# Kernel optimization log

Measured on AMD Instinct MI355X. Metric: run time of the kernel, lower is better.

The kernel has to match this reference:

```python
import jax, jax.numpy as jnp
import numpy as np

N_NODES = 10000
N_EDGES = 160000
B = 128
HEADS = 4
DIMS = [36, 128, 256, 512]
NEG_SLOPE = 0.2  # PyG GATConv default


def setup_inputs() -> dict:
    key = jax.random.key(0)
    ks = jax.random.split(key, 32)
    inp = {}
    inp["x"] = jax.random.normal(ks[0], (N_NODES, DIMS[0]), jnp.float32)
    inp["edge_index"] = jax.random.randint(ks[1], (2, N_EDGES), 0, N_NODES)
    inp["batch"] = jnp.sort(jax.random.randint(ks[2], (N_NODES,), 0, B))
    ki = 3
    for i in range(3):
        din, dout = DIMS[i], DIMS[i + 1]
        C = dout // HEADS
        inp[f"gcn_w{i}"] = jax.random.normal(ks[ki], (din, dout), jnp.float32) * (din ** -0.5); ki += 1
        inp[f"gcn_b{i}"] = jnp.zeros((dout,), jnp.float32)
        inp[f"gat_w{i}"] = jax.random.normal(ks[ki], (dout, dout), jnp.float32) * (dout ** -0.5); ki += 1
        inp[f"gat_as{i}"] = jax.random.normal(ks[ki], (HEADS, C), jnp.float32) * 0.1; ki += 1
        inp[f"gat_ad{i}"] = jax.random.normal(ks[ki], (HEADS, C), jnp.float32) * 0.1; ki += 1
        inp[f"gat_b{i}"] = jnp.zeros((dout,), jnp.float32)
    D = DIMS[-1]
    inp["ap_w1"] = jax.random.normal(ks[ki], (D, D // 2), jnp.float32) * (D ** -0.5); ki += 1
    inp["ap_b1"] = jnp.zeros((D // 2,), jnp.float32)
    inp["ap_w2"] = jax.random.normal(ks[ki], (D // 2, 1), jnp.float32) * ((D // 2) ** -0.5); ki += 1
    inp["ap_b2"] = jnp.zeros((1,), jnp.float32)
    return inp


def _gcn(x, w, b, src, dst, n):
    # PyG GCNConv: add self-loops, symmetric deg^-1/2 normalization, bias after agg
    h = x @ w  # [N, dout]
    deg = jax.ops.segment_sum(jnp.ones_like(dst, dtype=h.dtype), dst, n) + 1.0  # incl. self-loop
    dinv = deg ** -0.5
    norm = dinv[src] * dinv[dst]  # [E]
    agg = jax.ops.segment_sum(h[src] * norm[:, None], dst, n)
    agg = agg + h * (dinv * dinv)[:, None]  # self-loop messages
    return agg + b


def _gat(x, w, a_s, a_d, b, src, dst, n):
    # PyG GATConv: self-loops, leaky-relu logits, segment softmax over dst, concat heads
    C = w.shape[1] // HEADS
    h = (x @ w).reshape(n, HEADS, C)
    alpha_src = (h * a_s).sum(-1)  # [N, H]
    alpha_dst = (h * a_d).sum(-1)  # [N, H]
    loop = jnp.arange(n)
    s = jnp.concatenate([src, loop])
    d = jnp.concatenate([dst, loop])
    e = jax.nn.leaky_relu(alpha_src[s] + alpha_dst[d], NEG_SLOPE)  # [E+N, H]
    m = jax.ops.segment_max(e, d, n)
    ex = jnp.exp(e - m[d])
    den = jax.ops.segment_sum(ex, d, n)
    alpha = ex / den[d]  # [E+N, H]
    out = jax.ops.segment_sum(h[s] * alpha[:, :, None], d, n)  # [N, H, C]
    return out.reshape(n, HEADS * C) + b


def _forward(x, edge_index, batch, params, ap_w1, ap_b1, ap_w2, ap_b2):
    src, dst = edge_index[0], edge_index[1]
    n = x.shape[0]
    x_in = x
    n_layers = len(params)
    for i, (gw, gb, aw, a_s, a_d, ab) in enumerate(params):
        h = jax.nn.relu(_gcn(x, gw, gb, src, dst, n))  # dropout is identity in eval
        x = h + _gat(h, aw, a_s, a_d, ab, src, dst, n)
        if i < n_layers - 1:
            if x.shape[-1] == x_in.shape[-1]:
                x = x + x_in
            x_in = x
    # attention pooling (global softmax then per-graph masked renorm)
    a = jnp.tanh(x @ ap_w1 + ap_b1) @ ap_w2 + ap_b2  # [N, 1]
    a = jax.nn.softmax(a, axis=0)
    mask = jax.nn.one_hot(batch, B, dtype=x.dtype)  # [N, B]
    aw_ = a * mask
    aw_ = aw_ / (aw_.sum(0, keepdims=True) + 1e-8)
    graph_emb = aw_.T @ x  # [B, D]
    cnt = jax.ops.segment_sum(jnp.ones((n,), x.dtype), batch, B)
    ssum = jax.ops.segment_sum(x, batch, B)
    mean = ssum / jnp.maximum(cnt, 1.0)[:, None]
    smax = jax.ops.segment_max(x, batch, B)
    return jnp.concatenate([graph_emb, mean, smax, ssum], axis=1)  # [B, 4*D]


def reference(x, edge_index, batch,
              gcn_w0, gcn_b0, gat_w0, gat_as0, gat_ad0, gat_b0,
              gcn_w1, gcn_b1, gat_w1, gat_as1, gat_ad1, gat_b1,
              gcn_w2, gcn_b2, gat_w2, gat_as2, gat_ad2, gat_b2,
              ap_w1, ap_b1, ap_w2, ap_b2):
    params = [
        (gcn_w0, gcn_b0, gat_w0, gat_as0, gat_ad0, gat_b0),
        (gcn_w1, gcn_b1, gat_w1, gat_as1, gat_ad1, gat_b1),
        (gcn_w2, gcn_b2, gat_w2, gat_as2, gat_ad2, gat_b2),
    ]
    return _forward(x, edge_index, batch, params, ap_w1, ap_b1, ap_w2, ap_b2)
```

## Files before the change

kernel.cpp:

```cpp
#include <hip/hip_runtime.h>
#include <math.h>

#define NN 10000
#define NE 160000
#define NB 128
#define NH 4
#define DOUT 512
#define NEG 0.2f
#define SCAN_BLKS ((NN + 255) / 256)

typedef __attribute__((ext_vector_type(8))) short short8;
typedef __attribute__((ext_vector_type(4))) float f32x4;
typedef __attribute__((ext_vector_type(4))) unsigned short us4;

__device__ __forceinline__ float leakyf(float v){ return v > 0.f ? v : NEG*v; }
__device__ __forceinline__ void fma4(float4& a, const float4 v, float w){
  a.x += v.x*w; a.y += v.y*w; a.z += v.z*w; a.w += v.w*w;
}
__device__ __forceinline__ void mul4(float4& a, float s){
  a.x *= s; a.y *= s; a.z *= s; a.w *= s;
}
__device__ __forceinline__ unsigned short f2bf(float f){
  unsigned int u = __float_as_uint(f);
  u += 0x7FFFu + ((u >> 16) & 1u);
  return (unsigned short)(u >> 16);
}
__device__ __forceinline__ float bf2f(unsigned short h){
  return __uint_as_float(((unsigned int)h) << 16);
}
__device__ __forceinline__ void split2(float v, unsigned short& h, unsigned short& l){
  h = f2bf(v);
  l = f2bf(v - bf2f(h));
}
__device__ __forceinline__ void store_hl(unsigned short* H, unsigned short* L,
                                         size_t base, float4 v){
  us4 h, l; unsigned short hh, ll;
  split2(v.x, hh, ll); h[0]=hh; l[0]=ll;
  split2(v.y, hh, ll); h[1]=hh; l[1]=ll;
  split2(v.z, hh, ll); h[2]=hh; l[2]=ll;
  split2(v.w, hh, ll); h[3]=hh; l[3]=ll;
  *(us4*)&H[base] = h;
  *(us4*)&L[base] = l;
}
__device__ __forceinline__ float4 load_hl(const unsigned short* __restrict__ H,
                                          const unsigned short* __restrict__ L, size_t base){
  us4 h = *(const us4*)&H[base];
  us4 l = *(const us4*)&L[base];
  return make_float4(bf2f(h[0])+bf2f(l[0]), bf2f(h[1])+bf2f(l[1]),
                     bf2f(h[2])+bf2f(l[2]), bf2f(h[3])+bf2f(l[3]));
}
__device__ __forceinline__ void gl_lds16(const unsigned short* g, unsigned short* l){
  __builtin_amdgcn_global_load_lds(
      (const __attribute__((address_space(1))) unsigned int*)g,
      (__attribute__((address_space(3))) unsigned int*)l, 16, 0, 0);
}

__global__ void k_count(const int* __restrict__ dst, int* __restrict__ cnt){
  int e = blockIdx.x*blockDim.x + threadIdx.x;
  if (e < NE) atomicAdd(&cnt[dst[e]], 1);
}
__global__ void k_scan1(const int* __restrict__ cnt, int* __restrict__ bsum,
                        const int* __restrict__ batch, int* __restrict__ starts){
  __shared__ int red[256];
  int blk = blockIdx.x, t = threadIdx.x;
  int idx = blk*256 + t;
  red[t] = (idx < NN) ? cnt[idx] : 0;
  __syncthreads();
  for (int o = 128; o > 0; o >>= 1){
    if (t < o) red[t] += red[t + o];
    __syncthreads();
  }
  if (t == 0) bsum[blk] = red[0];
  if (blk == 0 && t <= NB){
    int lo = 0, hi = NN;
    while (lo < hi){ int mid = (lo + hi) >> 1; if (batch[mid] < t) lo = mid + 1; else hi = mid; }
    starts[t] = lo;
  }
}
__global__ void k_scan2(int* __restrict__ bsum, int* __restrict__ rowptr){
  if (threadIdx.x == 0){
    int acc = 0;
    for (int i = 0; i < SCAN_BLKS; i++){
      int c = bsum[i]; bsum[i] = acc; acc += c;
    }
    rowptr[NN] = acc;
  }
}
__global__ void k_scan3(const int* __restrict__ cnt, const int* __restrict__ bsum,
                        int* __restrict__ rowptr, float* __restrict__ dinv,
                        int* __restrict__ cursor, float* __restrict__ apre){
  __shared__ int s[256];
  int blk = blockIdx.x, t = threadIdx.x;
  int idx = blk*256 + t;
  int c = (idx < NN) ? cnt[idx] : 0;
  s[t] = c; __syncthreads();
  for (int o = 1; o < 256; o <<= 1){
    int v = 0;
    if (t >= o) v = s[t - o];
    __syncthreads();
    if (t >= o) s[t] += v;
    __syncthreads();
  }
  if (idx < NN){
    rowptr[idx] = bsum[blk] + s[t] - c;
    dinv[idx] = rsqrtf((float)c + 1.f);
    cursor[idx] = 0;
    apre[idx] = 0.f;
  }
}
__global__ void k_fill(const int* __restrict__ src, const int* __restrict__ dst,
                       const int* __restrict__ rowptr, int* __restrict__ cursor,
                       int* __restrict__ colidx){
  int e = blockIdx.x*blockDim.x + threadIdx.x;
  if (e >= NE) return;
  int d = dst[e];
  int pos = atomicAdd(&cursor[d], 1);
  colidx[rowptr[d] + pos] = src[e];
}

struct AllConv {
  const float* src[8];
  unsigned short* dh[8];
  unsigned short* dl[8];
  int K[8], Mm[8], Kp[8], tot[8];
};
__global__ void k_convall(AllConv a){
  int j = blockIdx.y;
  int idx = blockIdx.x*blockDim.x + threadIdx.x;
  if (idx >= a.tot[j]) return;
  float v;
  if (j == 0){
    int n = idx >> 6, c = idx & 63;
    v = (c < 36) ? a.src[0][n*36 + c] : 0.f;
  } else {
    int Kp = a.Kp[j], K = a.K[j], M = a.Mm[j];
    int kk = idx % Kp, m = idx / Kp;
    v = (kk < K) ? a.src[j][(size_t)kk*M + m] : 0.f;
  }
  unsigned short h, l; split2(v, h, l);
  a.dh[j][idx] = h; a.dl[j][idx] = l;
}

#define GBM 64
#define GBN 128
#define GBK 32
__global__ __launch_bounds__(256) void k_gemm_bf3(
    const unsigned short* __restrict__ Ah, const unsigned short* __restrict__ Al,
    const unsigned short* __restrict__ Bh, const unsigned short* __restrict__ Bl,
    float* __restrict__ C, int N, int Kp, int M, int mode,
    const float* __restrict__ bias, unsigned short* __restrict__ outH,
    unsigned short* __restrict__ outL,
    const float* __restrict__ a_s, const float* __restrict__ a_d,
    float* __restrict__ as_o, float* __restrict__ ad_o, int Cdim){
  __shared__ unsigned short AsH[GBM*GBK], AsL[GBM*GBK];
  __shared__ unsigned short BsH[GBN*GBK], BsL[GBN*GBK];
  __shared__ float sred[2][GBM][4];
  int gx = M / GBN;
  int gy = (N + GBM - 1) / GBM;
  const int G = 8;
  int bid = blockIdx.x;
  int full = gy / G;
  int bid_full = full * G * gx;
  int by, bx;
  if (bid < bid_full){
    int g = bid / (G*gx); int rem = bid % (G*gx);
    by = g*G + rem % G; bx = rem / G;
  } else {
    int rem = bid - bid_full; int rows = gy - full*G;
    by = full*G + rem % rows; bx = rem / rows;
  }
  int row0 = by * GBM, col0 = bx * GBN;
  int t = threadIdx.x;
  int w = t >> 6, L = t & 63;
  int lm = L & 15, lq = L >> 4;
  int wc = w * 32;

  int sr = L >> 2, sc = L & 3;
  int art = w*16 + sr;
  int ga  = (sc - ((art >> 1) & 3)) & 3;
  int agrow = min(row0 + art, N-1);
  int brt0 = w*16 + sr;
  int brt1 = (w+4)*16 + sr;
  int gb0 = (sc - ((brt0 >> 1) & 3)) & 3;
  int gb1 = (sc - ((brt1 >> 1) & 3)) & 3;
  int bgrow0 = col0 + brt0, bgrow1 = col0 + brt1;

  int rc = (lq + (lm >> 1)) & 3;
  int aoff[4], boff[2];
#pragma unroll
  for (int mi = 0; mi < 4; mi++) aoff[mi] = (mi*16 + lm)*32 + rc*8;
#pragma unroll
  for (int ni = 0; ni < 2; ni++) boff[ni] = (wc + ni*16 + lm)*32 + rc*8;

  f32x4 acc[4][2];
#pragma unroll
  for (int i = 0; i < 4; i++)
#pragma unroll
    for (int j = 0; j < 2; j++) acc[i][j] = (f32x4){0.f,0.f,0.f,0.f};

  int nk = Kp / GBK;
  for (int kt = 0; kt < nk; kt++){
    int k0 = kt * GBK;
    if (kt) __syncthreads();
    gl_lds16(&Ah[(size_t)agrow*Kp + k0 + ga*8],  &AsH[w*512]);
    gl_lds16(&Al[(size_t)agrow*Kp + k0 + ga*8],  &AsL[w*512]);
    gl_lds16(&Bh[(size_t)bgrow0*Kp + k0 + gb0*8], &BsH[w*512]);
    gl_lds16(&Bh[(size_t)bgrow1*Kp + k0 + gb1*8], &BsH[(w+4)*512]);
    gl_lds16(&Bl[(size_t)bgrow0*Kp + k0 + gb0*8], &BsL[w*512]);
    gl_lds16(&Bl[(size_t)bgrow1*Kp + k0 + gb1*8], &BsL[(w+4)*512]);
    __syncthreads();

    short8 ah[4], al[4], bh[2], bl[2];
#pragma unroll
    for (int mi = 0; mi < 4; mi++){
      ah[mi] = *(const short8*)&AsH[aoff[mi]];
      al[mi] = *(const short8*)&AsL[aoff[mi]];
    }
#pragma unroll
    for (int ni = 0; ni < 2; ni++){
      bh[ni] = *(const short8*)&BsH[boff[ni]];
      bl[ni] = *(const short8*)&BsL[boff[ni]];
    }
#pragma unroll
    for (int mi = 0; mi < 4; mi++)
#pragma unroll
      for (int ni = 0; ni < 2; ni++){
        acc[mi][ni] = __builtin_amdgcn_mfma_f32_16x16x32_bf16(ah[mi], bh[ni], acc[mi][ni], 0, 0, 0);
        acc[mi][ni] = __builtin_amdgcn_mfma_f32_16x16x32_bf16(ah[mi], bl[ni], acc[mi][ni], 0, 0, 0);
        acc[mi][ni] = __builtin_amdgcn_mfma_f32_16x16x32_bf16(al[mi], bh[ni], acc[mi][ni], 0, 0, 0);
      }
  }
  if (mode == 1){
#pragma unroll
    for (int mi = 0; mi < 4; mi++)
#pragma unroll
      for (int ni = 0; ni < 2; ni++){
#pragma unroll
        for (int r = 0; r < 4; r++){
          int row = row0 + mi*16 + lq*4 + r;
          int col = col0 + wc + ni*16 + lm;
          if (row < N){
            float v = fmaxf(acc[mi][ni][r] + bias[col], 0.f);
            unsigned short hh, ll; split2(v, hh, ll);
            outH[(size_t)row*M + col] = hh;
            outL[(size_t)row*M + col] = ll;
          }
        }
      }
  } else if (mode != 3){
#pragma unroll
    for (int mi = 0; mi < 4; mi++)
#pragma unroll
      for (int ni = 0; ni < 2; ni++){
#pragma unroll
        for (int r = 0; r < 4; r++){
          int row = row0 + mi*16 + lq*4 + r;
          int col = col0 + wc + ni*16 + lm;
          if (row < N) C[(size_t)row*M + col] = acc[mi][ni][r];
        }
      }
  }
  if (mode == 2){
    float sA0 = a_s[col0 + wc + lm], sA1 = a_s[col0 + wc + 16 + lm];
    float dA0 = a_d[col0 + wc + lm], dA1 = a_d[col0 + wc + 16 + lm];
#pragma unroll
    for (int mi = 0; mi < 4; mi++)
#pragma unroll
      for (int r = 0; r < 4; r++){
        float vs = acc[mi][0][r]*sA0 + acc[mi][1][r]*sA1;
        float vd = acc[mi][0][r]*dA0 + acc[mi][1][r]*dA1;
#pragma unroll
        for (int o = 1; o <= 8; o <<= 1){
          vs += __shfl_xor(vs, o);
          vd += __shfl_xor(vd, o);
        }
        if (lm == 0){
          int row = mi*16 + lq*4 + r;
          sred[0][row][w] = vs;
          sred[1][row][w] = vd;
        }
      }
    __syncthreads();
    if (t < GBM){
      int n = row0 + t;
      if (n < N){
        int wph = Cdim >> 5;
        int nheads = 4 / wph;
        for (int g = 0; g < nheads; g++){
          float ss = 0.f, dd = 0.f;
          for (int q = 0; q < wph; q++){
            ss += sred[0][t][g*wph + q];
            dd += sred[1][t][g*wph + q];
          }
          int hd = (col0 + g*wph*32) / Cdim;
          as_o[n*NH + hd] = ss;
          ad_o[n*NH + hd] = dd;
        }
      }
    }
  } else if (mode == 3){
    float b0 = bias[col0 + wc + lm], b1v = bias[col0 + wc + 16 + lm];
    float w0v = a_s[col0 + wc + lm], w1v = a_s[col0 + wc + 16 + lm];
#pragma unroll
    for (int mi = 0; mi < 4; mi++)
#pragma unroll
      for (int r = 0; r < 4; r++){
        float v = tanhf(acc[mi][0][r] + b0)*w0v + tanhf(acc[mi][1][r] + b1v)*w1v;
#pragma unroll
        for (int o = 1; o <= 8; o <<= 1) v += __shfl_xor(v, o);
        if (lm == 0) sred[0][mi*16 + lq*4 + r][w] = v;
      }
    __syncthreads();
    if (t < GBM){
      int n = row0 + t;
      if (n < N){
        float s = sred[0][t][0] + sred[0][t][1] + sred[0][t][2] + sred[0][t][3];
        atomicAdd(&as_o[n], s);
      }
    }
  }
}

__global__ __launch_bounds__(256) void k_gcn_pre(
    const unsigned short* __restrict__ inH, const unsigned short* __restrict__ inL,
    const float* __restrict__ dinv,
    const int* __restrict__ rowptr, const int* __restrict__ colidx,
    unsigned short* __restrict__ outH, unsigned short* __restrict__ outL,
    int Kp, int nchunk){
  int bid = blockIdx.x;
  int chunk = bid % nchunk, grp = bid / nchunk;
  int t = threadIdx.x;
  int sub = t & 15;
  int n = grp*16 + (t >> 4);
  if (n >= NN) return;
  int f0 = chunk*64 + sub*4;
  int b = rowptr[n], e = rowptr[n+1];
  float dn = dinv[n];
  float4 a0 = make_float4(0,0,0,0), a1 = make_float4(0,0,0,0);
  float4 a2 = make_float4(0,0,0,0), a3 = make_float4(0,0,0,0);
  int j = b;
  for (; j + 3 < e; j += 4){
    int s0 = colidx[j], s1 = colidx[j+1], s2 = colidx[j+2], s3 = colidx[j+3];
    float w0 = dinv[s0], w1 = dinv[s1], w2 = dinv[s2], w3 = dinv[s3];
    float4 v0 = load_hl(inH, inL, (size_t)s0*Kp + f0);
    float4 v1 = load_hl(inH, inL, (size_t)s1*Kp + f0);
    float4 v2 = load_hl(inH, inL, (size_t)s2*Kp + f0);
    float4 v3 = load_hl(inH, inL, (size_t)s3*Kp + f0);
    fma4(a0, v0, w0*dn); fma4(a1, v1, w1*dn);
    fma4(a2, v2, w2*dn); fma4(a3, v3, w3*dn);
  }
  for (; j < e; j++){
    int s = colidx[j];
    float4 v = load_hl(inH, inL, (size_t)s*Kp + f0);
    fma4(a0, v, dinv[s]*dn);
  }
  float4 acc = make_float4(a0.x+a1.x+a2.x+a3.x, a0.y+a1.y+a2.y+a3.y,
                           a0.z+a1.z+a2.z+a3.z, a0.w+a1.w+a2.w+a3.w);
  float4 sv = load_hl(inH, inL, (size_t)n*Kp + f0);
  float dn2 = dn*dn;
  acc.x += sv.x*dn2; acc.y += sv.y*dn2; acc.z += sv.z*dn2; acc.w += sv.w*dn2;
  store_hl(outH, outL, (size_t)n*Kp + f0, acc);
}

__global__ __launch_bounds__(256) void k_gat_gather(
    const float* __restrict__ hg,
    const unsigned short* __restrict__ inH, const unsigned short* __restrict__ inL,
    const int* __restrict__ rowptr, const int* __restrict__ colidx,
    const float* __restrict__ as_, const float* __restrict__ ad_,
    const float* __restrict__ ab,
    unsigned short* __restrict__ outH, unsigned short* __restrict__ outL,
    int M, int C, int nchunk){
  int bid = blockIdx.x;
  int chunk = bid % nchunk, grp = bid / nchunk;
  int t = threadIdx.x;
  int sub = t & 15;
  int n = grp*16 + (t >> 4);
  if (n >= NN) return;
  int f0 = chunk*64 + sub*4;
  int hd = f0 / C;
  int b = rowptr[n], e = rowptr[n+1];
  int ai = n*NH + hd;
  float adn = ad_[ai];
  float selflog = leakyf(as_[ai] + adn);
  float m = selflog, d = 1.f;
  float4 a0 = make_float4(0,0,0,0), a1 = make_float4(0,0,0,0);
  float4 a2 = make_float4(0,0,0,0), a3 = make_float4(0,0,0,0);
  int j = b;
  for (; j + 3 < e; j += 4){
    int s0 = colidx[j], s1 = colidx[j+1], s2 = colidx[j+2], s3 = colidx[j+3];
    float l0 = leakyf(as_[s0*NH + hd] + adn), l1 = leakyf(as_[s1*NH + hd] + adn);
    float l2 = leakyf(as_[s2*NH + hd] + adn), l3 = leakyf(as_[s3*NH + hd] + adn);
    float4 v0 = *(const float4*)&hg[(size_t)s0*M + f0];
    float4 v1 = *(const float4*)&hg[(size_t)s1*M + f0];
    float4 v2 = *(const float4*)&hg[(size_t)s2*M + f0];
    float4 v3 = *(const float4*)&hg[(size_t)s3*M + f0];
    float m4 = fmaxf(fmaxf(l0, l1), fmaxf(l2, l3));
    if (m4 > m){
      float sc = expf(m - m4);
      d *= sc; mul4(a0, sc); mul4(a1, sc); mul4(a2, sc); mul4(a3, sc);
      m = m4;
    }
    float w0 = expf(l0 - m), w1 = expf(l1 - m);
    float w2 = expf(l2 - m), w3 = expf(l3 - m);
    d += (w0 + w1) + (w2 + w3);
    fma4(a0, v0, w0); fma4(a1, v1, w1);
    fma4(a2, v2, w2); fma4(a3, v3, w3);
  }
  for (; j < e; j++){
    int s = colidx[j];
    float l = leakyf(as_[s*NH + hd] + adn);
    float4 v = *(const float4*)&hg[(size_t)s*M + f0];
    if (l > m){
      float sc = expf(m - l);
      d *= sc; mul4(a0, sc); mul4(a1, sc); mul4(a2, sc); mul4(a3, sc);
      m = l;
    }
    float ww = expf(l - m);
    d += ww;
    fma4(a0, v, ww);
  }
  float4 acc = make_float4(a0.x+a1.x+a2.x+a3.x, a0.y+a1.y+a2.y+a3.y,
                           a0.z+a1.z+a2.z+a3.z, a0.w+a1.w+a2.w+a3.w);
  float es = expf(selflog - m), inv = 1.f/d;
  float4 sv = *(const float4*)&hg[(size_t)n*M + f0];
  float4 hv = load_hl(inH, inL, (size_t)n*M + f0);
  float4 bb = *(const float4*)&ab[f0];
  float4 r = make_float4(
    hv.x + bb.x + (sv.x*es + acc.x)*inv,
    hv.y + bb.y + (sv.y*es + acc.y)*inv,
    hv.z + bb.z + (sv.z*es + acc.z)*inv,
    hv.w + bb.w + (sv.w*es + acc.w)*inv);
  store_hl(outH, outL, (size_t)n*M + f0, r);
}

__global__ void k_pool(const unsigned short* __restrict__ xH, const unsigned short* __restrict__ xL,
                       const float* __restrict__ apre, const int* __restrict__ starts,
                       float* __restrict__ out){
  __shared__ float red[128];
  int g = blockIdx.x, t = threadIdx.x;
  int b = starts[g], e = starts[g+1];
  float m = -INFINITY;
  for (int n = b + t; n < e; n += 128) m = fmaxf(m, apre[n]);
  red[t] = m; __syncthreads();
  for (int o = 64; o > 0; o >>= 1){
    if (t < o) red[t] = fmaxf(red[t], red[t + o]);
    __syncthreads();
  }
  m = red[0]; __syncthreads();
  float s = 0.f;
  for (int n = b + t; n < e; n += 128) s += expf(apre[n] - m);
  red[t] = s; __syncthreads();
  for (int o = 64; o > 0; o >>= 1){
    if (t < o) red[t] += red[t + o];
    __syncthreads();
  }
  float inv = 1.f / (red[0] + 1e-8f);
  float4 sum = make_float4(0,0,0,0), wacc = make_float4(0,0,0,0);
  float4 mx = make_float4(-INFINITY,-INFINITY,-INFINITY,-INFINITY);
  for (int n = b; n < e; n++){
    float4 xv = load_hl(xH, xL, (size_t)n*DOUT + t*4);
    float p = expf(apre[n] - m) * inv;
    sum.x += xv.x; sum.y += xv.y; sum.z += xv.z; sum.w += xv.w;
    mx.x = fmaxf(mx.x, xv.x); mx.y = fmaxf(mx.y, xv.y);
    mx.z = fmaxf(mx.z, xv.z); mx.w = fmaxf(mx.w, xv.w);
    fma4(wacc, xv, p);
  }
  float ic = 1.f / fmaxf((float)(e - b), 1.f);
  float4* o = (float4*)(out + (size_t)g*4*DOUT);
  o[t]       = wacc;
  o[128 + t] = make_float4(sum.x*ic, sum.y*ic, sum.z*ic, sum.w*ic);
  o[256 + t] = mx;
  o[384 + t] = sum;
}

extern "C" void kernel_launch(void* const* d_in, const int* in_sizes, int n_in,
                              void* d_out, int out_size, void* d_ws, size_t ws_size,
                              hipStream_t stream) {
  const float* x0   = (const float*)d_in[0];
  const int*   ei   = (const int*)d_in[1];
  const int*   src  = ei;
  const int*   dst  = ei + NE;
  const int*   batch= (const int*)d_in[2];
  const float* gw[3]  = {(const float*)d_in[3],  (const float*)d_in[9],  (const float*)d_in[15]};
  const float* gb[3]  = {(const float*)d_in[4],  (const float*)d_in[10], (const float*)d_in[16]};
  const float* aw[3]  = {(const float*)d_in[5],  (const float*)d_in[11], (const float*)d_in[17]};
  const float* asw[3] = {(const float*)d_in[6],  (const float*)d_in[12], (const float*)d_in[18]};
  const float* adw[3] = {(const float*)d_in[7],  (const float*)d_in[13], (const float*)d_in[19]};
  const float* ab[3]  = {(const float*)d_in[8],  (const float*)d_in[14], (const float*)d_in[20]};
  const float* apw1 = (const float*)d_in[21];
  const float* apb1 = (const float*)d_in[22];
  const float* apw2 = (const float*)d_in[23];
  float* out = (float*)d_out;

  char* p = (char*)d_ws;
  auto alloc = [&](size_t bytes) -> void* {
    void* r = (void*)p; p += (bytes + 255) & ~(size_t)255; return r;
  };
  float* f1 = (float*)alloc((size_t)NN*512*4);
  unsigned short* actH0 = (unsigned short*)alloc((size_t)NN*512*2);
  unsigned short* actL0 = (unsigned short*)alloc((size_t)NN*512*2);
  unsigned short* actH1 = (unsigned short*)alloc((size_t)NN*512*2);
  unsigned short* actL1 = (unsigned short*)alloc((size_t)NN*512*2);
  unsigned short* preH  = (unsigned short*)alloc((size_t)NN*256*2);
  unsigned short* preL  = (unsigned short*)alloc((size_t)NN*256*2);
  unsigned short* x0h = (unsigned short*)alloc((size_t)NN*64*2);
  unsigned short* x0l = (unsigned short*)alloc((size_t)NN*64*2);
  const int wK[7]  = {36, 128, 128, 256, 256, 512, 512};
  const int wM[7]  = {128, 128, 256, 256, 512, 512, 256};
  const int wKp[7] = {64, 128, 128, 256, 256, 512, 512};
  const float* wsrc[7] = {gw[0], aw[0], gw[1], aw[1], gw[2], aw[2], apw1};
  unsigned short* wTh[7]; unsigned short* wTl[7];
  for (int i = 0; i < 7; i++){
    size_t sz = (size_t)wM[i]*wKp[i]*2;
    wTh[i] = (unsigned short*)alloc(sz);
    wTl[i] = (unsigned short*)alloc(sz);
  }
  float* dinv = (float*)alloc(NN*4);
  float* as_  = (float*)alloc(NN*NH*4);
  float* ad_  = (float*)alloc(NN*NH*4);
  float* apre = (float*)alloc(NN*4);
  int* rowptr = (int*)alloc((NN+1)*4);
  int* colidx = (int*)alloc((size_t)NE*4);
  int* cnt    = (int*)alloc(NN*4);
  int* cursor = (int*)alloc(NN*4);
  int* starts = (int*)alloc((NB+1)*4);
  int* bsum   = (int*)alloc(SCAN_BLKS*4);

  hipMemsetAsync(cnt, 0, NN*sizeof(int), stream);
  k_count<<<(NE+255)/256, 256, 0, stream>>>(dst, cnt);
  k_scan1<<<SCAN_BLKS, 256, 0, stream>>>(cnt, bsum, batch, starts);
  k_scan2<<<1, 64, 0, stream>>>(bsum, rowptr);
  k_scan3<<<SCAN_BLKS, 256, 0, stream>>>(cnt, bsum, rowptr, dinv, cursor, apre);
  k_fill<<<(NE+255)/256, 256, 0, stream>>>(src, dst, rowptr, cursor, colidx);

  AllConv ac;
  ac.src[0] = x0; ac.dh[0] = x0h; ac.dl[0] = x0l;
  ac.K[0] = 36; ac.Mm[0] = NN; ac.Kp[0] = 64; ac.tot[0] = NN*64;
  int maxtot = NN*64;
  for (int i = 0; i < 7; i++){
    ac.src[i+1] = wsrc[i]; ac.dh[i+1] = wTh[i]; ac.dl[i+1] = wTl[i];
    ac.K[i+1] = wK[i]; ac.Mm[i+1] = wM[i]; ac.Kp[i+1] = wKp[i];
    ac.tot[i+1] = wKp[i]*wM[i];
    if (ac.tot[i+1] > maxtot) maxtot = ac.tot[i+1];
  }
  k_convall<<<dim3((maxtot+255)/256, 8), 256, 0, stream>>>(ac);

  const int dims[4] = {36, 128, 256, 512};
  const int ngrp = (NN + 15) / 16;
  const unsigned short* curH = x0h; const unsigned short* curL = x0l;
  int wi = 0;
  for (int i = 0; i < 3; i++){
    int Kin = (i == 0) ? 64 : dims[i];
    int M = dims[i+1], C = M/NH;
    int nchunk_in = Kin / 64;
    int nchunk = M / 64;
    int nblk = (M/GBN) * ((NN+GBM-1)/GBM);
    k_gcn_pre<<<nchunk_in*ngrp, 256, 0, stream>>>(curH, curL, dinv, rowptr, colidx,
                                                  preH, preL, Kin, nchunk_in);
    k_gemm_bf3<<<nblk, 256, 0, stream>>>(preH, preL, wTh[wi], wTl[wi], f1, NN, wKp[wi], M,
                                         1, gb[i], actH0, actL0,
                                         nullptr, nullptr, nullptr, nullptr, C);
    wi++;
    k_gemm_bf3<<<nblk, 256, 0, stream>>>(actH0, actL0, wTh[wi], wTl[wi], f1, NN, wKp[wi], M,
                                         2, nullptr, nullptr, nullptr,
                                         asw[i], adw[i], as_, ad_, C);
    wi++;
    k_gat_gather<<<nchunk*ngrp, 256, 0, stream>>>(f1, actH0, actL0, rowptr, colidx,
                                                  as_, ad_, ab[i],
                                                  actH1, actL1, M, C, nchunk);
    curH = actH1; curL = actL1;
  }

  {
    int nblk = (256/GBN) * ((NN+GBM-1)/GBM);
    k_gemm_bf3<<<nblk, 256, 0, stream>>>(actH1, actL1, wTh[6], wTl[6], f1, NN, wKp[6], 256,
                                         3, apb1, nullptr, nullptr,
                                         apw2, nullptr, apre, nullptr, 64);
  }
  k_pool<<<NB, 128, 0, stream>>>(actH1, actL1, apre, starts, out);
}
```

Before: 410.5 us.

## Merge setup kernels and aggregate first-layer input directly from fp32

Edge counting and the weight transpose/split conversion now run in one launch, dispatched by block index. The single-thread scan2 kernel is removed; each scan3 block sums the preceding block totals itself. The first GCN aggregation reads the fp32 input x directly and writes zeros to the padded columns, so the x0 bf16 split buffers and their conversion pass are dropped. This cuts three launches and one intermediate pass, at the cost of a serial prefix loop per block and a linear search over segments in the conversion path.

```diff
diff --git a/kernel.cpp b/kernel.cpp
--- a/kernel.cpp
+++ b/kernel.cpp
@@ -8,6 +8,7 @@
 #define DOUT 512
 #define NEG 0.2f
 #define SCAN_BLKS ((NN + 255) / 256)
+#define CNT_BLKS ((NE + 255) / 256)
 
 typedef __attribute__((ext_vector_type(8))) short short8;
 typedef __attribute__((ext_vector_type(4))) float f32x4;
@@ -55,9 +56,30 @@
       (__attribute__((address_space(3))) unsigned int*)l, 16, 0, 0);
 }
 
-__global__ void k_count(const int* __restrict__ dst, int* __restrict__ cnt){
-  int e = blockIdx.x*blockDim.x + threadIdx.x;
-  if (e < NE) atomicAdd(&cnt[dst[e]], 1);
+struct AllConv {
+  const float* src[7];
+  unsigned short* dh[7];
+  unsigned short* dl[7];
+  int K[7], Mm[7], Kp[7], tot[7];
+};
+
+__global__ void k_count_conv(const int* __restrict__ dst, int* __restrict__ cnt,
+                             AllConv a, int convTot){
+  int bid = blockIdx.x;
+  if (bid < CNT_BLKS){
+    int e = bid*256 + threadIdx.x;
+    if (e < NE) atomicAdd(&cnt[dst[e]], 1);
+  } else {
+    int idx = (bid - CNT_BLKS)*256 + threadIdx.x;
+    if (idx >= convTot) return;
+    int j = 0;
+    while (idx >= a.tot[j]){ idx -= a.tot[j]; j++; }
+    int Kp = a.Kp[j], K = a.K[j], M = a.Mm[j];
+    int kk = idx % Kp, m = idx / Kp;
+    float v = (kk < K) ? a.src[j][(size_t)kk*M + m] : 0.f;
+    unsigned short h, l; split2(v, h, l);
+    a.dh[j][idx] = h; a.dl[j][idx] = l;
+  }
 }
 __global__ void k_scan1(const int* __restrict__ cnt, int* __restrict__ bsum,
                         const int* __restrict__ batch, int* __restrict__ starts){
@@ -77,23 +99,26 @@
     starts[t] = lo;
   }
 }
-__global__ void k_scan2(int* __restrict__ bsum, int* __restrict__ rowptr){
-  if (threadIdx.x == 0){
-    int acc = 0;
-    for (int i = 0; i < SCAN_BLKS; i++){
-      int c = bsum[i]; bsum[i] = acc; acc += c;
-    }
-    rowptr[NN] = acc;
-  }
-}
 __global__ void k_scan3(const int* __restrict__ cnt, const int* __restrict__ bsum,
                         int* __restrict__ rowptr, float* __restrict__ dinv,
                         int* __restrict__ cursor, float* __restrict__ apre){
   __shared__ int s[256];
+  __shared__ int base_s;
   int blk = blockIdx.x, t = threadIdx.x;
   int idx = blk*256 + t;
   int c = (idx < NN) ? cnt[idx] : 0;
-  s[t] = c; __syncthreads();
+  s[t] = c;
+  if (t == 0){
+    int acc = 0;
+    for (int i = 0; i < blk; i++) acc += bsum[i];
+    base_s = acc;
+    if (blk == SCAN_BLKS - 1){
+      int tot = acc;
+      for (int i = blk; i < SCAN_BLKS; i++) tot += bsum[i];
+      rowptr[NN] = tot;
+    }
+  }
+  __syncthreads();
   for (int o = 1; o < 256; o <<= 1){
     int v = 0;
     if (t >= o) v = s[t - o];
@@ -102,7 +127,7 @@
     __syncthreads();
   }
   if (idx < NN){
-    rowptr[idx] = bsum[blk] + s[t] - c;
+    rowptr[idx] = base_s + s[t] - c;
     dinv[idx] = rsqrtf((float)c + 1.f);
     cursor[idx] = 0;
     apre[idx] = 0.f;
@@ -116,29 +141,6 @@
   int d = dst[e];
   int pos = atomicAdd(&cursor[d], 1);
   colidx[rowptr[d] + pos] = src[e];
-}
-
-struct AllConv {
-  const float* src[8];
-  unsigned short* dh[8];
-  unsigned short* dl[8];
-  int K[8], Mm[8], Kp[8], tot[8];
-};
-__global__ void k_convall(AllConv a){
-  int j = blockIdx.y;
-  int idx = blockIdx.x*blockDim.x + threadIdx.x;
-  if (idx >= a.tot[j]) return;
-  float v;
-  if (j == 0){
-    int n = idx >> 6, c = idx & 63;
-    v = (c < 36) ? a.src[0][n*36 + c] : 0.f;
-  } else {
-    int Kp = a.Kp[j], K = a.K[j], M = a.Mm[j];
-    int kk = idx % Kp, m = idx / Kp;
-    v = (kk < K) ? a.src[j][(size_t)kk*M + m] : 0.f;
-  }
-  unsigned short h, l; split2(v, h, l);
-  a.dh[j][idx] = h; a.dl[j][idx] = l;
 }
 
 #define GBM 64
@@ -319,6 +321,48 @@
       }
     }
   }
+}
+
+__global__ __launch_bounds__(256) void k_gcn_pre0(
+    const float* __restrict__ x0, const float* __restrict__ dinv,
+    const int* __restrict__ rowptr, const int* __restrict__ colidx,
+    unsigned short* __restrict__ outH, unsigned short* __restrict__ outL){
+  int t = threadIdx.x;
+  int sub = t & 15;
+  int n = blockIdx.x*16 + (t >> 4);
+  if (n >= NN) return;
+  int f0 = sub*4;
+  bool act = f0 < 36;
+  int b = rowptr[n], e = rowptr[n+1];
+  float dn = dinv[n];
+  float4 a0 = make_float4(0,0,0,0), a1 = make_float4(0,0,0,0);
+  float4 a2 = make_float4(0,0,0,0), a3 = make_float4(0,0,0,0);
+  if (act){
+    int j = b;
+    for (; j + 3 < e; j += 4){
+      int s0 = colidx[j], s1 = colidx[j+1], s2 = colidx[j+2], s3 = colidx[j+3];
+      float w0 = dinv[s0], w1 = dinv[s1], w2 = dinv[s2], w3 = dinv[s3];
+      float4 v0 = *(const float4*)&x0[(size_t)s0*36 + f0];
+      float4 v1 = *(const float4*)&x0[(size_t)s1*36 + f0];
+      float4 v2 = *(const float4*)&x0[(size_t)s2*36 + f0];
+      float4 v3 = *(const float4*)&x0[(size_t)s3*36 + f0];
+      fma4(a0, v0, w0*dn); fma4(a1, v1, w1*dn);
+      fma4(a2, v2, w2*dn); fma4(a3, v3, w3*dn);
+    }
+    for (; j < e; j++){
+      int s = colidx[j];
+      float4 v = *(const float4*)&x0[(size_t)s*36 + f0];
+      fma4(a0, v, dinv[s]*dn);
+    }
+  }
+  float4 acc = make_float4(a0.x+a1.x+a2.x+a3.x, a0.y+a1.y+a2.y+a3.y,
+                           a0.z+a1.z+a2.z+a3.z, a0.w+a1.w+a2.w+a3.w);
+  if (act){
+    float4 sv = *(const float4*)&x0[(size_t)n*36 + f0];
+    float dn2 = dn*dn;
+    acc.x += sv.x*dn2; acc.y += sv.y*dn2; acc.z += sv.z*dn2; acc.w += sv.w*dn2;
+  }
+  store_hl(outH, outL, (size_t)n*64 + f0, acc);
 }
 
 __global__ __launch_bounds__(256) void k_gcn_pre(
@@ -503,8 +547,6 @@
   unsigned short* actL1 = (unsigned short*)alloc((size_t)NN*512*2);
   unsigned short* preH  = (unsigned short*)alloc((size_t)NN*256*2);
   unsigned short* preL  = (unsigned short*)alloc((size_t)NN*256*2);
-  unsigned short* x0h = (unsigned short*)alloc((size_t)NN*64*2);
-  unsigned short* x0l = (unsigned short*)alloc((size_t)NN*64*2);
   const int wK[7]  = {36, 128, 128, 256, 256, 512, 512};
   const int wM[7]  = {128, 128, 256, 256, 512, 512, 256};
   const int wKp[7] = {64, 128, 128, 256, 256, 512, 512};
@@ -526,28 +568,25 @@
   int* starts = (int*)alloc((NB+1)*4);
   int* bsum   = (int*)alloc(SCAN_BLKS*4);
 
+  AllConv ac;
+  int convTot = 0;
+  for (int i = 0; i < 7; i++){
+    ac.src[i] = wsrc[i]; ac.dh[i] = wTh[i]; ac.dl[i] = wTl[i];
+    ac.K[i] = wK[i]; ac.Mm[i] = wM[i]; ac.Kp[i] = wKp[i];
+    ac.tot[i] = wKp[i]*wM[i];
+    convTot += ac.tot[i];
+  }
+
   hipMemsetAsync(cnt, 0, NN*sizeof(int), stream);
-  k_count<<<(NE+255)/256, 256, 0, stream>>>(dst, cnt);
+  int convBlks = (convTot + 255) / 256;
+  k_count_conv<<<CNT_BLKS + convBlks, 256, 0, stream>>>(dst, cnt, ac, convTot);
   k_scan1<<<SCAN_BLKS, 256, 0, stream>>>(cnt, bsum, batch, starts);
-  k_scan2<<<1, 64, 0, stream>>>(bsum, rowptr);
   k_scan3<<<SCAN_BLKS, 256, 0, stream>>>(cnt, bsum, rowptr, dinv, cursor, apre);
   k_fill<<<(NE+255)/256, 256, 0, stream>>>(src, dst, rowptr, cursor, colidx);
 
-  AllConv ac;
-  ac.src[0] = x0; ac.dh[0] = x0h; ac.dl[0] = x0l;
-  ac.K[0] = 36; ac.Mm[0] = NN; ac.Kp[0] = 64; ac.tot[0] = NN*64;
-  int maxtot = NN*64;
-  for (int i = 0; i < 7; i++){
-    ac.src[i+1] = wsrc[i]; ac.dh[i+1] = wTh[i]; ac.dl[i+1] = wTl[i];
-    ac.K[i+1] = wK[i]; ac.Mm[i+1] = wM[i]; ac.Kp[i+1] = wKp[i];
-    ac.tot[i+1] = wKp[i]*wM[i];
-    if (ac.tot[i+1] > maxtot) maxtot = ac.tot[i+1];
-  }
-  k_convall<<<dim3((maxtot+255)/256, 8), 256, 0, stream>>>(ac);
-
   const int dims[4] = {36, 128, 256, 512};
   const int ngrp = (NN + 15) / 16;
-  const unsigned short* curH = x0h; const unsigned short* curL = x0l;
+  const unsigned short* curH = nullptr; const unsigned short* curL = nullptr;
   int wi = 0;
   for (int i = 0; i < 3; i++){
     int Kin = (i == 0) ? 64 : dims[i];
@@ -555,8 +594,12 @@
     int nchunk_in = Kin / 64;
     int nchunk = M / 64;
     int nblk = (M/GBN) * ((NN+GBM-1)/GBM);
-    k_gcn_pre<<<nchunk_in*ngrp, 256, 0, stream>>>(curH, curL, dinv, rowptr, colidx,
-                                                  preH, preL, Kin, nchunk_in);
+    if (i == 0){
+      k_gcn_pre0<<<ngrp, 256, 0, stream>>>(x0, dinv, rowptr, colidx, preH, preL);
+    } else {
+      k_gcn_pre<<<nchunk_in*ngrp, 256, 0, stream>>>(curH, curL, dinv, rowptr, colidx,
+                                                    preH, preL, Kin, nchunk_in);
+    }
     k_gemm_bf3<<<nblk, 256, 0, stream>>>(preH, preL, wTh[wi], wTl[wi], f1, NN, wKp[wi], M,
                                          1, gb[i], actH0, actL0,
                                          nullptr, nullptr, nullptr, nullptr, C);
```

Measured after the change: 399.1 us (median of 2 runs). -2.8%, faster.
